# Kernel optimization log

Hardware: AMD Instinct MI355X
Metric: run time of the kernel (lower is better)

Reference implementation:

```python
import jax, jax.numpy as jnp
import numpy as np

N = 50000      # num nodes
E = 1_600_000  # num edges
D = 64         # in_dim == hidden_dim
H = 4          # heads
C = 16         # head_dim = hidden_dim // heads
NEG = 0.2      # leaky_relu negative slope (PyG GATConv default)


def setup_inputs() -> dict:
    key = jax.random.key(0)
    ks = jax.random.split(key, 20)
    f = lambda k, s: (jax.random.normal(k, s, jnp.float32) * 0.1)
    return dict(
        node_features=jax.random.normal(ks[0], (N, D), jnp.float32),
        edge_index=jax.random.randint(ks[1], (2, E), 0, N, dtype=jnp.int32),
        edge_type=jax.random.randint(ks[2], (E,), 0, 5, dtype=jnp.int32),
        edge_attr=jax.random.normal(ks[3], (E, 1), jnp.float32),
        # GAT layer 1 (PyG GATConv: lin has no bias, att_* are [H,C], final bias [H*C])
        W1=f(ks[4], (D, H * C)), att_src1=f(ks[5], (H, C)), att_dst1=f(ks[6], (H, C)),
        We1=f(ks[7], (1, H * C)), att_e1=f(ks[8], (H, C)), b1=jnp.zeros((H * C,), jnp.float32),
        # GAT layer 2
        W2=f(ks[9], (D, H * C)), att_src2=f(ks[10], (H, C)), att_dst2=f(ks[11], (H, C)),
        We2=f(ks[12], (1, H * C)), att_e2=f(ks[13], (H, C)), b2=jnp.zeros((H * C,), jnp.float32),
        # LayerNorms
        g1=jnp.ones((D,), jnp.float32), beta1=jnp.zeros((D,), jnp.float32),
        g2=jnp.ones((D,), jnp.float32), beta2=jnp.zeros((D,), jnp.float32),
        # output head
        Wout=f(ks[14], (D, 1)), bout=jnp.zeros((1,), jnp.float32),
    )


def _layernorm(x, g, b, eps=1e-5):
    mu = x.mean(-1, keepdims=True)
    v = ((x - mu) ** 2).mean(-1, keepdims=True)
    return (x - mu) * jax.lax.rsqrt(v + eps) * g + b


def _seg_softmax(alpha, dst, n):
    # numerically stable segment softmax over incoming edges of each dst node
    m = jax.ops.segment_max(alpha, dst, num_segments=n)
    m = jnp.where(jnp.isfinite(m), m, 0.0)
    ex = jnp.exp(alpha - m[dst])
    den = jax.ops.segment_sum(ex, dst, num_segments=n)
    return ex / (den[dst] + 1e-16)


def _gatconv(x, src, dst, eattr, W, a_s, a_d, We, a_e, b, n):
    xs = (x @ W).reshape(n, H, C)                       # [N,H,C]
    a_src = jnp.einsum('nhc,hc->nh', xs, a_s)           # [N,H]
    a_dst = jnp.einsum('nhc,hc->nh', xs, a_d)           # [N,H]
    ee = (eattr @ We).reshape(-1, H, C)                 # [E',H,C]
    a_edge = jnp.einsum('ehc,hc->eh', ee, a_e)          # [E',H]
    alpha = a_src[src] + a_dst[dst] + a_edge            # [E',H]
    alpha = jax.nn.leaky_relu(alpha, NEG)
    alpha = _seg_softmax(alpha, dst, n)                 # [E',H]
    msg = xs[src] * alpha[..., None]                    # [E',H,C] gather-weighted messages
    out = jax.ops.segment_sum(msg, dst, num_segments=n) # scatter-aggregate
    return out.reshape(n, H * C) + b


def reference(node_features, edge_index, edge_type, edge_attr,
              W1, att_src1, att_dst1, We1, att_e1, b1,
              W2, att_src2, att_dst2, We2, att_e2, b2,
              g1, beta1, g2, beta2, Wout, bout):
    src, dst = edge_index[0], edge_index[1]
    # PyG add_self_loops(fill_value='mean'): self-loop edge_attr = mean of edge_attr over incoming edges
    cnt = jax.ops.segment_sum(jnp.ones((E,), jnp.float32), dst, num_segments=N)
    loop_attr = jax.ops.segment_sum(edge_attr, dst, num_segments=N) / jnp.maximum(cnt, 1.0)[:, None]
    loops = jnp.arange(N, dtype=src.dtype)
    src2 = jnp.concatenate([src, loops])
    dst2 = jnp.concatenate([dst, loops])
    ea = jnp.concatenate([edge_attr, loop_attr], axis=0)

    residual = node_features  # in_dim == hidden_dim -> no res_proj
    h = _gatconv(node_features, src2, dst2, ea, W1, att_src1, att_dst1, We1, att_e1, b1, N)
    h = jax.nn.elu(_layernorm(h + residual, g1, beta1))
    residual = h
    h = _gatconv(h, src2, dst2, ea, W2, att_src2, att_dst2, We2, att_e2, b2, N)
    h = jax.nn.elu(_layernorm(h + residual, g2, beta2))
    return h @ Wout + bout
```

## Files before the change

kernel.cpp:

```cpp
#include <hip/hip_runtime.h>
#include <hip/hip_bf16.h>
#include <cfloat>

#define NN 50000
#define NE 1600000
#define NEG 0.2f
#define NBKT 392
#define BNODE 128
#define P1_TILE 2048
#define P1_BLOCKS 782
#define CAP 16
#define BCAP 4608
#define SLOTS 96
#define L2E 1.4426950408889634f

typedef __attribute__((ext_vector_type(8))) short bf8_t;
typedef __attribute__((ext_vector_type(4))) float f4_t;

__device__ __forceinline__ float bf16bits_to_f(unsigned v) {
  return __uint_as_float(v << 16);
}
__device__ __forceinline__ unsigned f_to_bf16bits(float f) {
  unsigned u = __float_as_uint(f);
  return (u + 0x7fffu + ((u >> 16) & 1u)) >> 16;
}

__global__ __launch_bounds__(256) void bin_kernel(
    const int* __restrict__ src, const int* __restrict__ dst,
    const float* __restrict__ ea, int* __restrict__ gcnt,
    int2* __restrict__ gbuf) {
  __shared__ int lcnt[NBKT];
  __shared__ int lbase[NBKT];
  __shared__ int2 lbuf[NBKT][CAP];
  int t = threadIdx.x;
  for (int i = t; i < NBKT; i += 256) lcnt[i] = 0;
  __syncthreads();
  int e0 = blockIdx.x * P1_TILE;
#pragma unroll
  for (int k = 0; k < P1_TILE / 256; ++k) {
    int e = e0 + k * 256 + t;
    if (e < NE) {
      int d = dst[e];
      int b = d >> 7;
      int2 v = make_int2(((d & 127) << 16) | src[e], __float_as_int(ea[e]));
      int pos = atomicAdd(&lcnt[b], 1);
      if (pos < CAP) {
        lbuf[b][pos] = v;
      } else {
        int gp = atomicAdd(&gcnt[b], 1);
        if (gp < BCAP) gbuf[(size_t)b * BCAP + gp] = v;
      }
    }
  }
  __syncthreads();
  for (int i = t; i < NBKT; i += 256) {
    int len = lcnt[i]; if (len > CAP) len = CAP;
    lbase[i] = atomicAdd(&gcnt[i], len);
  }
  __syncthreads();
  for (int sid = t; sid < NBKT * CAP; sid += 256) {
    int b = sid >> 4;
    int k = sid & (CAP - 1);
    int len = lcnt[b]; if (len > CAP) len = CAP;
    if (k < len) {
      int base = lbase[b];
      if (base + k < BCAP) gbuf[(size_t)b * BCAP + base + k] = lbuf[b][k];
    }
  }
}

__global__ __launch_bounds__(256) void build_kernel(
    const int* __restrict__ gcnt, const int2* __restrict__ gbuf,
    int* __restrict__ cnt, unsigned* __restrict__ csr) {
  __shared__ int lc[BNODE];
  int t = threadIdx.x;
  int b = blockIdx.x;
  if (t < BNODE) lc[t] = 0;
  __syncthreads();
  int len = gcnt[b]; if (len > BCAP) len = BCAP;
  const int2* buf = gbuf + (size_t)b * BCAP;
  for (int i = t; i < len; i += 256) {
    int2 v = buf[i];
    int dl = (v.x >> 16) & 127;
    int s = v.x & 0xffff;
    int pos = atomicAdd(&lc[dl], 1);
    if (pos < SLOTS) {
      unsigned eb = ((unsigned)v.y) & 0xffff0000u;
      csr[(size_t)(b * BNODE + dl) * SLOTS + pos] = eb | (unsigned)s;
    }
  }
  __syncthreads();
  if (t < BNODE) {
    int n = b * BNODE + t;
    if (n < NN) cnt[n] = min(lc[t], SLOTS);
  }
}

__device__ __forceinline__ bf8_t pack8(const float* p) {
  bf8_t r;
#pragma unroll
  for (int i = 0; i < 8; ++i) r[i] = (short)f_to_bf16bits(p[i]);
  return r;
}

template <bool FP32IN>
__global__ __launch_bounds__(256) void gemm_mfma_kernel(
    const void* __restrict__ xin, const float* __restrict__ W,
    const float* __restrict__ att_s, const float* __restrict__ att_d,
    unsigned short* __restrict__ xsb, float* __restrict__ a_src,
    float* __restrict__ a_dst) {
  __shared__ unsigned short Wt[64][68];
  int t = threadIdx.x;
  for (int i = t; i < 4096; i += 256) {
    int k = i >> 6, n = i & 63;
    Wt[n][k] = (unsigned short)f_to_bf16bits(W[i]);
  }
  __syncthreads();
  int lane = t & 63, wave = t >> 6;
  int quad = lane >> 4, n16 = lane & 15;

  bf8_t bfrag[4][2];
#pragma unroll
  for (int nt = 0; nt < 4; ++nt)
#pragma unroll
    for (int kk = 0; kk < 2; ++kk)
      bfrag[nt][kk] = *(const bf8_t*)&Wt[nt * 16 + n16][kk * 32 + quad * 8];

  float as4[4], ad4[4];
#pragma unroll
  for (int nt = 0; nt < 4; ++nt) {
    as4[nt] = att_s[nt * 16 + n16];
    ad4[nt] = att_d[nt * 16 + n16];
  }

  int r0w = blockIdx.x * 128 + wave * 32;
#pragma unroll
  for (int tile = 0; tile < 2; ++tile) {
    int r0 = r0w + tile * 16;
    int rowA = r0 + n16; if (rowA > NN - 1) rowA = NN - 1;
    bf8_t af0, af1;
    if (FP32IN) {
      const float* xr = (const float*)xin + (size_t)rowA * 64 + quad * 8;
      af0 = pack8(xr);
      af1 = pack8(xr + 32);
    } else {
      const bf8_t* xrow =
          (const bf8_t*)((const unsigned short*)xin + (size_t)rowA * 64);
      af0 = xrow[quad];
      af1 = xrow[4 + quad];
    }
#pragma unroll
    for (int nt = 0; nt < 4; ++nt) {
      f4_t acc = {0.f, 0.f, 0.f, 0.f};
      acc = __builtin_amdgcn_mfma_f32_16x16x32_bf16(af0, bfrag[nt][0], acc, 0, 0, 0);
      acc = __builtin_amdgcn_mfma_f32_16x16x32_bf16(af1, bfrag[nt][1], acc, 0, 0, 0);
#pragma unroll
      for (int reg = 0; reg < 4; ++reg) {
        int row = r0 + quad * 4 + reg;
        float v = acc[reg];
        if (row < NN)
          xsb[(size_t)row * 64 + nt * 16 + n16] = (unsigned short)f_to_bf16bits(v);
        float p = v * as4[nt];
        float q = v * ad4[nt];
#pragma unroll
        for (int off = 8; off; off >>= 1) {
          p += __shfl_xor(p, off, 16);
          q += __shfl_xor(q, off, 16);
        }
        if (n16 == 0 && row < NN) {
          a_src[row * 4 + nt] = p * L2E;
          a_dst[row * 4 + nt] = q * L2E;
        }
      }
    }
  }
}

template <bool HEAD>
__global__ __launch_bounds__(256) void aggregate_kernel(
    const int* __restrict__ cnt, const unsigned* __restrict__ csr,
    const unsigned short* __restrict__ xsb, const float* __restrict__ a_src,
    const float* __restrict__ a_dst, const float* __restrict__ We,
    const float* __restrict__ att_e, const float* __restrict__ bias,
    const float* __restrict__ res, const float* __restrict__ g,
    const float* __restrict__ beta, const float* __restrict__ Wout,
    const float* __restrict__ bout, float* __restrict__ out,
    unsigned short* __restrict__ out_b) {
  __shared__ __align__(16) uint2 rec[4][64][4];
  int t = threadIdx.x;
  int lane = t & 63, wave = t >> 6;
  int n = blockIdx.x * 4 + wave;
  int d2 = lane & 31;
  int hb = d2 >> 3;
  int half = lane >> 5;

  float sp = We[lane] * att_e[lane];
#pragma unroll
  for (int off = 8; off; off >>= 1) sp += __shfl_xor(sp, off, 16);
  sp *= L2E;
  float s0 = __shfl(sp, 0, 64), s1 = __shfl(sp, 16, 64);
  float s2 = __shfl(sp, 32, 64), s3 = __shfl(sp, 48, 64);

  const float4 adv = *(const float4*)(a_dst + (size_t)n * 4);

  int dn = cnt[n];
  int r0 = n * SLOTS, r1 = r0 + dn;
  float accx = 0.f, accy = 0.f, den = 0.f, easum = 0.f;
  const uint2* rpb = &rec[wave][half][hb];
  const char* xd = (const char*)xsb + d2 * 4;

  for (int base = r0; base < r1; base += 64) {
    int c = r1 - base; if (c > 64) c = 64;
    int e = base + lane;
    unsigned ce = (e < r1) ? csr[e] : 0u;
    float ea = __uint_as_float(ce & 0xffff0000u);
    easum += ea;
    unsigned soff = (ce & 0xffffu) * 128u;
    float ex0 = 0.f, ex1 = 0.f, ex2 = 0.f, ex3 = 0.f;
    if (e < r1) {
      const float4 av = *(const float4*)(a_src + (size_t)(ce & 0xffffu) * 4);
      float a0 = av.x + fmaf(ea, s0, adv.x); a0 = fmaxf(a0, NEG * a0);
      float a1 = av.y + fmaf(ea, s1, adv.y); a1 = fmaxf(a1, NEG * a1);
      float a2 = av.z + fmaf(ea, s2, adv.z); a2 = fmaxf(a2, NEG * a2);
      float a3 = av.w + fmaf(ea, s3, adv.w); a3 = fmaxf(a3, NEG * a3);
      ex0 = exp2f(a0); ex1 = exp2f(a1); ex2 = exp2f(a2); ex3 = exp2f(a3);
    }
    uint4* wp = (uint4*)&rec[wave][lane][0];
    wp[0] = make_uint4(soff, __float_as_uint(ex0), soff, __float_as_uint(ex1));
    wp[1] = make_uint4(soff, __float_as_uint(ex2), soff, __float_as_uint(ex3));
    int c4 = (c + 3) & ~3;
    for (int j = 0; j < c4; j += 4) {
      uint2 va = rpb[j * 4];
      uint2 vb = rpb[j * 4 + 8];
      unsigned ua = *(const unsigned*)(xd + va.x);
      unsigned ub = *(const unsigned*)(xd + vb.x);
      float efa = __uint_as_float(va.y), efb = __uint_as_float(vb.y);
      den += efa + efb;
      accx = fmaf(efa, __uint_as_float(ua << 16), accx);
      accy = fmaf(efa, __uint_as_float(ua & 0xffff0000u), accy);
      accx = fmaf(efb, __uint_as_float(ub << 16), accx);
      accy = fmaf(efb, __uint_as_float(ub & 0xffff0000u), accy);
    }
  }

  den += __shfl_xor(den, 32, 64);
  accx += __shfl_xor(accx, 32, 64);
  accy += __shfl_xor(accy, 32, 64);
#pragma unroll
  for (int off = 32; off; off >>= 1) easum += __shfl_xor(easum, off, 64);

  float loop_ea = easum / fmaxf((float)dn, 1.0f);
  float as_h = a_src[(size_t)n * 4 + hb];
  float adn = (hb == 0) ? adv.x : (hb == 1) ? adv.y : (hb == 2) ? adv.z : adv.w;
  float sph = (hb == 0) ? s0 : (hb == 1) ? s1 : (hb == 2) ? s2 : s3;
  float a_self = as_h + fmaf(loop_ea, sph, adn);
  a_self = fmaxf(a_self, NEG * a_self);
  float ex_self = exp2f(a_self);
  den += ex_self;
  unsigned un = *(const unsigned*)((const char*)xsb + (size_t)n * 128 + d2 * 4);
  accx = fmaf(ex_self, __uint_as_float(un << 16), accx);
  accy = fmaf(ex_self, __uint_as_float(un & 0xffff0000u), accy);

  float rden = 1.f / (den + 1e-16f);
  const float2 bi = *(const float2*)(bias + d2 * 2);
  const float2 rsd = *(const float2*)(res + (size_t)n * 64 + d2 * 2);
  float vx = accx * rden + bi.x + rsd.x;
  float vy = accy * rden + bi.y + rsd.y;
  float s = vx + vy;
#pragma unroll
  for (int off = 32; off; off >>= 1) s += __shfl_xor(s, off, 64);
  float mu = s * (1.0f / 128.0f);
  float dx = vx - mu, dy = vy - mu;
  float var = dx * dx + dy * dy;
#pragma unroll
  for (int off = 32; off; off >>= 1) var += __shfl_xor(var, off, 64);
  var *= (1.0f / 128.0f);
  float rstd = rsqrtf(var + 1e-5f);
  const float2 gg = *(const float2*)(g + d2 * 2);
  const float2 bb = *(const float2*)(beta + d2 * 2);
  float yx = dx * rstd * gg.x + bb.x;
  float yy = dy * rstd * gg.y + bb.y;
  yx = yx > 0.f ? yx : expm1f(yx);
  yy = yy > 0.f ? yy : expm1f(yy);
  if (HEAD) {
    const float2 wv = *(const float2*)(Wout + d2 * 2);
    float p = yx * wv.x + yy * wv.y;
#pragma unroll
    for (int off = 32; off; off >>= 1) p += __shfl_xor(p, off, 64);
    if (lane == 0) out[n] = p * 0.5f + bout[0];
  } else if (lane < 32) {
    *(float2*)(out + (size_t)n * 64 + d2 * 2) = make_float2(yx, yy);
    unsigned ob = f_to_bf16bits(yx) | (f_to_bf16bits(yy) << 16);
    *(unsigned*)(out_b + (size_t)n * 64 + d2 * 2) = ob;
  }
}

extern "C" void kernel_launch(void* const* d_in, const int* in_sizes, int n_in,
                              void* d_out, int out_size, void* d_ws,
                              size_t ws_size, hipStream_t stream) {
  const float* node_features = (const float*)d_in[0];
  const int* edge_index = (const int*)d_in[1];
  const int* src = edge_index;
  const int* dst = edge_index + NE;
  const float* edge_attr = (const float*)d_in[3];
  const float* W1 = (const float*)d_in[4];
  const float* att_src1 = (const float*)d_in[5];
  const float* att_dst1 = (const float*)d_in[6];
  const float* We1 = (const float*)d_in[7];
  const float* att_e1 = (const float*)d_in[8];
  const float* b1 = (const float*)d_in[9];
  const float* W2 = (const float*)d_in[10];
  const float* att_src2 = (const float*)d_in[11];
  const float* att_dst2 = (const float*)d_in[12];
  const float* We2 = (const float*)d_in[13];
  const float* att_e2 = (const float*)d_in[14];
  const float* b2 = (const float*)d_in[15];
  const float* g1 = (const float*)d_in[16];
  const float* beta1 = (const float*)d_in[17];
  const float* g2 = (const float*)d_in[18];
  const float* beta2 = (const float*)d_in[19];
  const float* Wout = (const float*)d_in[20];
  const float* bout = (const float*)d_in[21];
  float* out = (float*)d_out;

  char* ws = (char*)d_ws;
  size_t o = 0;
  auto alloc = [&](size_t bytes) {
    void* p = ws + o;
    o += (bytes + 255) & ~(size_t)255;
    return p;
  };
  int* gcnt = (int*)alloc((size_t)NBKT * 4);
  int2* gbuf = (int2*)alloc((size_t)NBKT * BCAP * 8);
  int* cnt = (int*)alloc((size_t)NN * 4);
  unsigned* csr = (unsigned*)alloc((size_t)NN * SLOTS * 4);
  unsigned short* xsb = (unsigned short*)alloc((size_t)NN * 64 * 2);
  unsigned short* h1b = (unsigned short*)alloc((size_t)NN * 64 * 2);
  float* a_srcb = (float*)alloc((size_t)NN * 4 * 4);
  float* a_dstb = (float*)alloc((size_t)NN * 4 * 4);
  float* h1 = (float*)alloc((size_t)NN * 64 * 4);

  hipMemsetAsync(gcnt, 0, (size_t)NBKT * 4, stream);

  bin_kernel<<<P1_BLOCKS, 256, 0, stream>>>(src, dst, edge_attr, gcnt, gbuf);
  build_kernel<<<NBKT, 256, 0, stream>>>(gcnt, gbuf, cnt, csr);

  gemm_mfma_kernel<true><<<391, 256, 0, stream>>>(
      node_features, W1, att_src1, att_dst1, xsb, a_srcb, a_dstb);
  aggregate_kernel<false><<<NN / 4, 256, 0, stream>>>(
      cnt, csr, xsb, a_srcb, a_dstb, We1, att_e1, b1, node_features, g1, beta1,
      nullptr, nullptr, h1, h1b);

  gemm_mfma_kernel<false><<<391, 256, 0, stream>>>(
      h1b, W2, att_src2, att_dst2, xsb, a_srcb, a_dstb);
  aggregate_kernel<true><<<NN / 4, 256, 0, stream>>>(
      cnt, csr, xsb, a_srcb, a_dstb, We2, att_e2, b2, h1, g2, beta2, Wout, bout,
      out, nullptr);
}
```

Before: 277.3 us.

## Halve edge bucket size and split attention dots into separate kernel

Edge binning now uses 64-node buckets with smaller per-block tiles and local caps, which doubles the block count for bin and build and reduces per-bucket contention. The attention source/destination dot products move out of the MFMA GEMM epilogue into a new kernel that reads the bf16 projected features. This removes the shuffle reductions from the GEMM and lets it run one tile per wave across more blocks. The cost is two extra launches, an extra pass over the features, and dots computed from bf16-rounded values.

Result: slower. 297.9 us (+7.4%).

```diff
diff --git a/kernel.cpp b/kernel.cpp
--- a/kernel.cpp
+++ b/kernel.cpp
@@ -5,12 +5,12 @@
 #define NN 50000
 #define NE 1600000
 #define NEG 0.2f
-#define NBKT 392
-#define BNODE 128
-#define P1_TILE 2048
-#define P1_BLOCKS 782
-#define CAP 16
-#define BCAP 4608
+#define NBKT 782
+#define BNODE 64
+#define P1_TILE 1024
+#define P1_BLOCKS 1563
+#define CAP 4
+#define BCAP 2560
 #define SLOTS 96
 #define L2E 1.4426950408889634f
 
@@ -41,8 +41,8 @@
     int e = e0 + k * 256 + t;
     if (e < NE) {
       int d = dst[e];
-      int b = d >> 7;
-      int2 v = make_int2(((d & 127) << 16) | src[e], __float_as_int(ea[e]));
+      int b = d >> 6;
+      int2 v = make_int2(((d & 63) << 16) | src[e], __float_as_int(ea[e]));
       int pos = atomicAdd(&lcnt[b], 1);
       if (pos < CAP) {
         lbuf[b][pos] = v;
@@ -59,7 +59,7 @@
   }
   __syncthreads();
   for (int sid = t; sid < NBKT * CAP; sid += 256) {
-    int b = sid >> 4;
+    int b = sid >> 2;
     int k = sid & (CAP - 1);
     int len = lcnt[b]; if (len > CAP) len = CAP;
     if (k < len) {
@@ -81,7 +81,7 @@
   const int2* buf = gbuf + (size_t)b * BCAP;
   for (int i = t; i < len; i += 256) {
     int2 v = buf[i];
-    int dl = (v.x >> 16) & 127;
+    int dl = (v.x >> 16) & 63;
     int s = v.x & 0xffff;
     int pos = atomicAdd(&lc[dl], 1);
     if (pos < SLOTS) {
@@ -106,9 +106,7 @@
 template <bool FP32IN>
 __global__ __launch_bounds__(256) void gemm_mfma_kernel(
     const void* __restrict__ xin, const float* __restrict__ W,
-    const float* __restrict__ att_s, const float* __restrict__ att_d,
-    unsigned short* __restrict__ xsb, float* __restrict__ a_src,
-    float* __restrict__ a_dst) {
+    unsigned short* __restrict__ xsb) {
   __shared__ unsigned short Wt[64][68];
   int t = threadIdx.x;
   for (int i = t; i < 4096; i += 256) {
@@ -126,54 +124,58 @@
     for (int kk = 0; kk < 2; ++kk)
       bfrag[nt][kk] = *(const bf8_t*)&Wt[nt * 16 + n16][kk * 32 + quad * 8];
 
-  float as4[4], ad4[4];
+  int r0 = blockIdx.x * 64 + wave * 16;
+  int rowA = r0 + n16; if (rowA > NN - 1) rowA = NN - 1;
+  bf8_t af0, af1;
+  if (FP32IN) {
+    const float* xr = (const float*)xin + (size_t)rowA * 64 + quad * 8;
+    af0 = pack8(xr);
+    af1 = pack8(xr + 32);
+  } else {
+    const bf8_t* xrow =
+        (const bf8_t*)((const unsigned short*)xin + (size_t)rowA * 64);
+    af0 = xrow[quad];
+    af1 = xrow[4 + quad];
+  }
 #pragma unroll
   for (int nt = 0; nt < 4; ++nt) {
-    as4[nt] = att_s[nt * 16 + n16];
-    ad4[nt] = att_d[nt * 16 + n16];
-  }
-
-  int r0w = blockIdx.x * 128 + wave * 32;
-#pragma unroll
-  for (int tile = 0; tile < 2; ++tile) {
-    int r0 = r0w + tile * 16;
-    int rowA = r0 + n16; if (rowA > NN - 1) rowA = NN - 1;
-    bf8_t af0, af1;
-    if (FP32IN) {
-      const float* xr = (const float*)xin + (size_t)rowA * 64 + quad * 8;
-      af0 = pack8(xr);
-      af1 = pack8(xr + 32);
-    } else {
-      const bf8_t* xrow =
-          (const bf8_t*)((const unsigned short*)xin + (size_t)rowA * 64);
-      af0 = xrow[quad];
-      af1 = xrow[4 + quad];
-    }
-#pragma unroll
-    for (int nt = 0; nt < 4; ++nt) {
-      f4_t acc = {0.f, 0.f, 0.f, 0.f};
-      acc = __builtin_amdgcn_mfma_f32_16x16x32_bf16(af0, bfrag[nt][0], acc, 0, 0, 0);
-      acc = __builtin_amdgcn_mfma_f32_16x16x32_bf16(af1, bfrag[nt][1], acc, 0, 0, 0);
-#pragma unroll
-      for (int reg = 0; reg < 4; ++reg) {
-        int row = r0 + quad * 4 + reg;
-        float v = acc[reg];
-        if (row < NN)
-          xsb[(size_t)row * 64 + nt * 16 + n16] = (unsigned short)f_to_bf16bits(v);
-        float p = v * as4[nt];
-        float q = v * ad4[nt];
-#pragma unroll
-        for (int off = 8; off; off >>= 1) {
-          p += __shfl_xor(p, off, 16);
-          q += __shfl_xor(q, off, 16);
-        }
-        if (n16 == 0 && row < NN) {
-          a_src[row * 4 + nt] = p * L2E;
-          a_dst[row * 4 + nt] = q * L2E;
-        }
-      }
-    }
-  }
+    f4_t acc = {0.f, 0.f, 0.f, 0.f};
+    acc = __builtin_amdgcn_mfma_f32_16x16x32_bf16(af0, bfrag[nt][0], acc, 0, 0, 0);
+    acc = __builtin_amdgcn_mfma_f32_16x16x32_bf16(af1, bfrag[nt][1], acc, 0, 0, 0);
+#pragma unroll
+    for (int reg = 0; reg < 4; ++reg) {
+      int row = r0 + quad * 4 + reg;
+      if (row < NN)
+        xsb[(size_t)row * 64 + nt * 16 + n16] =
+            (unsigned short)f_to_bf16bits(acc[reg]);
+    }
+  }
+}
+
+__global__ __launch_bounds__(256) void att_dots_kernel(
+    const unsigned short* __restrict__ xsb, const float* __restrict__ att_s,
+    const float* __restrict__ att_d, float* __restrict__ a_src,
+    float* __restrict__ a_dst) {
+  int t = threadIdx.x;
+  int lane = t & 63, wave = t >> 6;
+  int n = blockIdx.x * 64 + wave * 16 + (lane >> 2);
+  int h = lane & 3;
+  if (n >= NN) return;
+  const uint4* xp = (const uint4*)(xsb + (size_t)n * 64 + h * 16);
+  uint4 w0 = xp[0], w1 = xp[1];
+  const float* as = att_s + h * 16;
+  const float* ad = att_d + h * 16;
+  unsigned dw[8] = {w0.x, w0.y, w0.z, w0.w, w1.x, w1.y, w1.z, w1.w};
+  float p = 0.f, q = 0.f;
+#pragma unroll
+  for (int c = 0; c < 8; ++c) {
+    float lo = bf16bits_to_f(dw[c] & 0xffffu);
+    float hi = __uint_as_float(dw[c] & 0xffff0000u);
+    p = fmaf(lo, as[2 * c], p); p = fmaf(hi, as[2 * c + 1], p);
+    q = fmaf(lo, ad[2 * c], q); q = fmaf(hi, ad[2 * c + 1], q);
+  }
+  a_src[n * 4 + h] = p * L2E;
+  a_dst[n * 4 + h] = q * L2E;
 }
 
 template <bool HEAD>
@@ -345,14 +347,16 @@
   bin_kernel<<<P1_BLOCKS, 256, 0, stream>>>(src, dst, edge_attr, gcnt, gbuf);
   build_kernel<<<NBKT, 256, 0, stream>>>(gcnt, gbuf, cnt, csr);
 
-  gemm_mfma_kernel<true><<<391, 256, 0, stream>>>(
-      node_features, W1, att_src1, att_dst1, xsb, a_srcb, a_dstb);
+  gemm_mfma_kernel<true><<<782, 256, 0, stream>>>(node_features, W1, xsb);
+  att_dots_kernel<<<782, 256, 0, stream>>>(xsb, att_src1, att_dst1, a_srcb,
+                                           a_dstb);
   aggregate_kernel<false><<<NN / 4, 256, 0, stream>>>(
       cnt, csr, xsb, a_srcb, a_dstb, We1, att_e1, b1, node_features, g1, beta1,
       nullptr, nullptr, h1, h1b);
 
-  gemm_mfma_kernel<false><<<391, 256, 0, stream>>>(
-      h1b, W2, att_src2, att_dst2, xsb, a_srcb, a_dstb);
+  gemm_mfma_kernel<false><<<782, 256, 0, stream>>>(h1b, W2, xsb);
+  att_dots_kernel<<<782, 256, 0, stream>>>(xsb, att_src2, att_dst2, a_srcb,
+                                           a_dstb);
   aggregate_kernel<true><<<NN / 4, 256, 0, stream>>>(
       cnt, csr, xsb, a_srcb, a_dstb, We2, att_e2, b2, h1, g2, beta2, Wout, bout,
       out, nullptr);
```
